# Kernel tuning notes

Measured on AMD Instinct MI355X. Metric: run time of the kernel, lower is better.

The kernel has to match this reference:

```python
import jax, jax.numpy as jnp
import numpy as np

B = 524288
N = 30
BETA = 3.0
MAX_A = 5.0

def setup_inputs() -> dict:
    key = jax.random.key(0)
    ks = jax.random.split(key, 10)
    return {
        "s":   jax.random.normal(ks[0], (B, 10), jnp.float32),
        "a":   jax.random.normal(ks[1], (B, 2), jnp.float32),
        "W1":  jax.random.normal(ks[2], (10, 100), jnp.float32) * 0.3,
        "b1":  jax.random.normal(ks[3], (100,), jnp.float32) * 0.1,
        "W2":  jax.random.normal(ks[4], (100, 30), jnp.float32) * 0.1,
        "b2":  jax.random.normal(ks[5], (30,), jnp.float32) * 0.1,
        "L1":  jax.random.normal(ks[6], (10, 100), jnp.float32) * 0.3,
        "bl1": jax.random.normal(ks[7], (100,), jnp.float32) * 0.1,
        "WL2": jax.random.normal(ks[8], (N, 100, 2), jnp.float32) * 0.1,
        "bL2": jax.random.normal(ks[9], (N, 2), jnp.float32) * 0.1,
    }

def reference(s, a, W1, b1, W2, b2, L1, bl1, WL2, bL2):
    # value branch: relu MLP -> per-centroid values [B, N]
    hv = jax.nn.relu(s @ W1 + b1)
    values = hv @ W2 + b2
    # location branch: relu MLP, then N fused tiny linears -> centroids [B, N, 2]
    hl = jax.nn.relu(s @ L1 + bl1)
    centroids = MAX_A * jnp.tanh(jnp.einsum('bh,nhd->bnd', hl, WL2) + bL2)
    # RBF weights: softmax over negated L2 distance to action, scaled by beta
    diff = centroids - a[:, None, :]          # [B, N, 2]
    dist = jnp.sqrt(jnp.sum(diff * diff, axis=2))  # [B, N]
    w = jax.nn.softmax(-BETA * dist, axis=1)
    # weighted sum of centroid values -> [B, 1]
    return jnp.sum(w * values, axis=1, keepdims=True)
```

## Files before the change

### kernel.cpp

```cpp
#include <hip/hip_runtime.h>
#include <hip/hip_fp16.h>


typedef _Float16 f16x8 __attribute__((ext_vector_type(8)));
typedef __fp16 fp16x2 __attribute__((ext_vector_type(2)));
typedef float f32x16 __attribute__((ext_vector_type(16)));
typedef unsigned u32x2 __attribute__((ext_vector_type(2)));

#define OFF_G1 0
#define OFF_WV 4096
#define OFF_WC 7680
#define TOT_HALVES 14848

__device__ __forceinline__ unsigned pkrtz_relu(float a, float b) {
    fp16x2 v = __builtin_amdgcn_cvt_pkrtz(a, b);
    fp16x2 z = {(__fp16)0.f, (__fp16)0.f};
    fp16x2 r = __builtin_elementwise_max(v, z);
    union { fp16x2 v; unsigned u; } U;
    U.v = r;
    return U.u;
}
__device__ __forceinline__ unsigned pk_rne(float a, float b) {
    union { __half h[2]; unsigned u; } U;
    U.h[0] = __float2half(a);
    U.h[1] = __float2half(b);
    return U.u;
}
__device__ __forceinline__ float tanh_fast(float x) {
    float e = exp2f(2.8853900817779268f * x);
    return 1.f - 2.f * __builtin_amdgcn_rcpf(e + 1.f);
}

__global__ __launch_bounds__(256) void prep_kernel(
    const float* __restrict__ W1, const float* __restrict__ b1,
    const float* __restrict__ W2, const float* __restrict__ b2,
    const float* __restrict__ L1, const float* __restrict__ bl1,
    const float* __restrict__ WL2, const float* __restrict__ bL2,
    unsigned short* __restrict__ ws)
{
    int idx = blockIdx.x * 256 + threadIdx.x;
    if (idx >= TOT_HALVES) return;
    float val = 0.f;

    if (idx < OFF_WV) {
        int r = idx >> 11, t = (idx >> 9) & 3;
        int ln = (idx >> 3) & 63, j = idx & 7;
        int c = 32 * t + (ln & 31);
        int k = (ln >> 5) * 8 + j;
        const float* W  = (r == 0) ? W1 : L1;
        const float* bb = (r == 0) ? b1 : bl1;
        if (c < 100)       val = (k < 10) ? W[k * 100 + c] : ((k == 10) ? bb[c] : 0.f);
        else if (c == 100) val = (k == 10) ? 1.f : 0.f;
    } else if (idx < OFF_WC) {
        int i = idx - OFF_WV;
        int kt = i >> 9, ln = (i >> 3) & 63, j = i & 7;
        int v = ln & 31;
        int n = (v & 0x19) | ((v & 4) >> 1) | ((v & 2) << 1);
        int k = kt * 16 + (ln >> 5) * 8 + j;
        if (n < 30) val = (k < 100) ? W2[k * 30 + n] : ((k == 100) ? b2[n] : 0.f);
    } else {
        int i = idx - OFF_WC;
        int T = i / 3584, rem = i % 3584;
        int kt = rem >> 9, ln = (rem >> 3) & 63, j = rem & 7;
        int row = ln & 31;
        int n = 16 * T + (row >> 1), d = row & 1;
        int k = kt * 16 + (ln >> 5) * 8 + j;
        if (n < 30) val = (k < 100) ? WL2[(n * 100 + k) * 2 + d]
                                    : ((k == 100) ? bL2[n * 2 + d] : 0.f);
    }
    union { __half h; unsigned short u; } cv;
    cv.h = __float2half(val);
    ws[idx] = cv.u;
}

__global__ __launch_bounds__(512, 4) void fused_kernel(
    const float* __restrict__ s, const float* __restrict__ a,
    const unsigned short* __restrict__ ws, float* __restrict__ out)
{
    __shared__ unsigned short lds[TOT_HALVES];
    const int tid  = threadIdx.x;
    const int lane = tid & 63;
    const int wave = tid >> 6;
    const int m32  = lane & 31;
    const int hi   = lane >> 5;
    const int sample = blockIdx.x * 256 + wave * 32 + m32;

    {
        const int4* g4 = (const int4*)ws;
        int4* l4 = (int4*)lds;
        for (int i = tid; i < TOT_HALVES / 8; i += 512) l4[i] = g4[i];
    }

    union Frag { f16x8 v; unsigned u[4]; };
    const f32x16 z16 = {0,0,0,0, 0,0,0,0, 0,0,0,0, 0,0,0,0};

    f16x8 sf;
    {
        Frag H;
        H.u[0] = 0; H.u[1] = 0; H.u[2] = 0; H.u[3] = 0;
        const float2* p = (const float2*)(s + (size_t)sample * 10);
        if (hi == 0) {
            float2 q0 = p[0], q1 = p[1], q2 = p[2], q3 = p[3];
            H.u[0] = pk_rne(q0.x, q0.y);
            H.u[1] = pk_rne(q1.x, q1.y);
            H.u[2] = pk_rne(q2.x, q2.y);
            H.u[3] = pk_rne(q3.x, q3.y);
        } else {
            float2 q4 = p[4];
            H.u[0] = pk_rne(q4.x, q4.y);
            H.u[1] = 0x00003C00u;
        }
        sf = H.v;
    }
    float2 av = ((const float2*)a)[sample];

    __syncthreads();

    f32x16 DV = z16, DC0 = z16, DC1 = z16;

    #pragma unroll
    for (int t = 0; t < 4; ++t) {
        f16x8 aV = *(const f16x8*)(lds + OFF_G1 + (0 * 4 + t) * 512 + lane * 8);
        f16x8 aH = *(const f16x8*)(lds + OFF_G1 + (1 * 4 + t) * 512 + lane * 8);
        f32x16 dv = __builtin_amdgcn_mfma_f32_32x32x16_f16(aV, sf, z16, 0, 0, 0);
        f32x16 dh = __builtin_amdgcn_mfma_f32_32x32x16_f16(aH, sf, z16, 0, 0, 0);

        unsigned qv[8], qh[8];
        #pragma unroll
        for (int q = 0; q < 8; ++q) {
            qv[q] = pkrtz_relu(dv[2 * q], dv[2 * q + 1]);
            qh[q] = pkrtz_relu(dh[2 * q], dh[2 * q + 1]);
        }

        #pragma unroll
        for (int half = 0; half < 2; ++half) {
            const int kt = 2 * t + half;
            if (kt < 7) {
                u32x2 sv0 = __builtin_amdgcn_permlane32_swap(qv[4*half+0], qv[4*half+2], false, false);
                u32x2 sv1 = __builtin_amdgcn_permlane32_swap(qv[4*half+1], qv[4*half+3], false, false);
                u32x2 sh0 = __builtin_amdgcn_permlane32_swap(qh[4*half+0], qh[4*half+2], false, false);
                u32x2 sh1 = __builtin_amdgcn_permlane32_swap(qh[4*half+1], qh[4*half+3], false, false);
                Frag BV, BH;
                BV.u[0] = sv0.x; BV.u[1] = sv1.x; BV.u[2] = sv0.y; BV.u[3] = sv1.y;
                BH.u[0] = sh0.x; BH.u[1] = sh1.x; BH.u[2] = sh0.y; BH.u[3] = sh1.y;

                f16x8 wv  = *(const f16x8*)(lds + OFF_WV + kt * 512 + lane * 8);
                f16x8 wc0 = *(const f16x8*)(lds + OFF_WC + (0 * 7 + kt) * 512 + lane * 8);
                f16x8 wc1 = *(const f16x8*)(lds + OFF_WC + (1 * 7 + kt) * 512 + lane * 8);
                DV  = __builtin_amdgcn_mfma_f32_32x32x16_f16(wv,  BV.v, DV,  0, 0, 0);
                DC0 = __builtin_amdgcn_mfma_f32_32x32x16_f16(wc0, BH.v, DC0, 0, 0, 0);
                DC1 = __builtin_amdgcn_mfma_f32_32x32x16_f16(wc1, BH.v, DC1, 0, 0, 0);
            }
        }
    }

    {
        float num = 0.f, den = 0.f;
        #pragma unroll
        for (int T = 0; T < 2; ++T) {
            #pragma unroll
            for (int q = 0; q < 8; ++q) {
                float cx = (T == 0) ? DC0[2 * q]     : DC1[2 * q];
                float cy = (T == 0) ? DC0[2 * q + 1] : DC1[2 * q + 1];
                float x = 5.f * tanh_fast(cx);
                float y = 5.f * tanh_fast(cy);
                float ex = x - av.x, ey = y - av.y;
                float dist = __builtin_amdgcn_sqrtf(fmaf(ex, ex, ey * ey));
                float wt = exp2f(-4.328085122666891f * dist);
                if (T == 1 && hi == 1 && q >= 6) wt = 0.f;
                num = fmaf(wt, DV[q + 8 * T], num);
                den += wt;
            }
        }
        num += __shfl_xor(num, 32);
        den += __shfl_xor(den, 32);
        if (lane < 32) out[sample] = num * __builtin_amdgcn_rcpf(den);
    }
}

extern "C" void kernel_launch(void* const* d_in, const int* in_sizes, int n_in,
                              void* d_out, int out_size, void* d_ws, size_t ws_size,
                              hipStream_t stream) {
    const float* s   = (const float*)d_in[0];
    const float* a   = (const float*)d_in[1];
    const float* W1  = (const float*)d_in[2];
    const float* b1  = (const float*)d_in[3];
    const float* W2  = (const float*)d_in[4];
    const float* b2  = (const float*)d_in[5];
    const float* L1  = (const float*)d_in[6];
    const float* bl1 = (const float*)d_in[7];
    const float* WL2 = (const float*)d_in[8];
    const float* bL2 = (const float*)d_in[9];
    float* out = (float*)d_out;
    unsigned short* ws = (unsigned short*)d_ws;

    prep_kernel<<<(TOT_HALVES + 255) / 256, 256, 0, stream>>>(
        W1, b1, W2, b2, L1, bl1, WL2, bL2, ws);

    int Btot = out_size;
    int grid = Btot / 256;
    fused_kernel<<<grid, 512, 0, stream>>>(s, a, ws, out);
}
```

Measured before the change: 38.80 us.

## Process two 32-sample tiles per wave to reuse LDS weight fragments

Each wave now handles 64 samples as two independent 32-sample MFMA tiles. Every weight fragment loaded from LDS feeds two MFMAs, and the grid is halved, so the per-block LDS weight copy is paid half as often. The cost is twice the accumulator and fragment registers per wave, with launch bounds relaxed from 4 to 2 blocks per CU, which may lower occupancy.

```diff
diff --git a/kernel.cpp b/kernel.cpp
--- a/kernel.cpp
+++ b/kernel.cpp
@@ -73,7 +73,7 @@
     ws[idx] = cv.u;
 }
 
-__global__ __launch_bounds__(512, 4) void fused_kernel(
+__global__ __launch_bounds__(512, 2) void fused_kernel(
     const float* __restrict__ s, const float* __restrict__ a,
     const unsigned short* __restrict__ ws, float* __restrict__ out)
 {
@@ -83,7 +83,9 @@
     const int wave = tid >> 6;
     const int m32  = lane & 31;
     const int hi   = lane >> 5;
-    const int sample = blockIdx.x * 256 + wave * 32 + m32;
+    const int base = blockIdx.x * 512 + wave * 64;
+    const int sA = base + m32;
+    const int sB = base + 32 + m32;
 
     {
         const int4* g4 = (const int4*)ws;
@@ -94,8 +96,7 @@
     union Frag { f16x8 v; unsigned u[4]; };
     const f32x16 z16 = {0,0,0,0, 0,0,0,0, 0,0,0,0, 0,0,0,0};
 
-    f16x8 sf;
-    {
+    auto loadS = [&](int sample) -> f16x8 {
         Frag H;
         H.u[0] = 0; H.u[1] = 0; H.u[2] = 0; H.u[3] = 0;
         const float2* p = (const float2*)(s + (size_t)sample * 10);
@@ -110,51 +111,76 @@
             H.u[0] = pk_rne(q4.x, q4.y);
             H.u[1] = 0x00003C00u;
         }
-        sf = H.v;
-    }
-    float2 av = ((const float2*)a)[sample];
+        return H.v;
+    };
+    f16x8 sfA = loadS(sA);
+    f16x8 sfB = loadS(sB);
+    float2 avA = ((const float2*)a)[sA];
+    float2 avB = ((const float2*)a)[sB];
 
     __syncthreads();
 
-    f32x16 DV = z16, DC0 = z16, DC1 = z16;
+    f32x16 DVA = z16, DC0A = z16, DC1A = z16;
+    f32x16 DVB = z16, DC0B = z16, DC1B = z16;
 
     #pragma unroll
     for (int t = 0; t < 4; ++t) {
-        f16x8 aV = *(const f16x8*)(lds + OFF_G1 + (0 * 4 + t) * 512 + lane * 8);
-        f16x8 aH = *(const f16x8*)(lds + OFF_G1 + (1 * 4 + t) * 512 + lane * 8);
-        f32x16 dv = __builtin_amdgcn_mfma_f32_32x32x16_f16(aV, sf, z16, 0, 0, 0);
-        f32x16 dh = __builtin_amdgcn_mfma_f32_32x32x16_f16(aH, sf, z16, 0, 0, 0);
-
-        unsigned qv[8], qh[8];
-        #pragma unroll
-        for (int q = 0; q < 8; ++q) {
-            qv[q] = pkrtz_relu(dv[2 * q], dv[2 * q + 1]);
-            qh[q] = pkrtz_relu(dh[2 * q], dh[2 * q + 1]);
+        unsigned qvA[8], qhA[8], qvB[8], qhB[8];
+        {
+            f16x8 aV = *(const f16x8*)(lds + OFF_G1 + (0 * 4 + t) * 512 + lane * 8);
+            f32x16 dvA = __builtin_amdgcn_mfma_f32_32x32x16_f16(aV, sfA, z16, 0, 0, 0);
+            f32x16 dvB = __builtin_amdgcn_mfma_f32_32x32x16_f16(aV, sfB, z16, 0, 0, 0);
+            #pragma unroll
+            for (int q = 0; q < 8; ++q) {
+                qvA[q] = pkrtz_relu(dvA[2 * q], dvA[2 * q + 1]);
+                qvB[q] = pkrtz_relu(dvB[2 * q], dvB[2 * q + 1]);
+            }
+        }
+        {
+            f16x8 aH = *(const f16x8*)(lds + OFF_G1 + (1 * 4 + t) * 512 + lane * 8);
+            f32x16 dhA = __builtin_amdgcn_mfma_f32_32x32x16_f16(aH, sfA, z16, 0, 0, 0);
+            f32x16 dhB = __builtin_amdgcn_mfma_f32_32x32x16_f16(aH, sfB, z16, 0, 0, 0);
+            #pragma unroll
+            for (int q = 0; q < 8; ++q) {
+                qhA[q] = pkrtz_relu(dhA[2 * q], dhA[2 * q + 1]);
+                qhB[q] = pkrtz_relu(dhB[2 * q], dhB[2 * q + 1]);
+            }
         }
 
         #pragma unroll
         for (int half = 0; half < 2; ++half) {
             const int kt = 2 * t + half;
             if (kt < 7) {
-                u32x2 sv0 = __builtin_amdgcn_permlane32_swap(qv[4*half+0], qv[4*half+2], false, false);
-                u32x2 sv1 = __builtin_amdgcn_permlane32_swap(qv[4*half+1], qv[4*half+3], false, false);
-                u32x2 sh0 = __builtin_amdgcn_permlane32_swap(qh[4*half+0], qh[4*half+2], false, false);
-                u32x2 sh1 = __builtin_amdgcn_permlane32_swap(qh[4*half+1], qh[4*half+3], false, false);
-                Frag BV, BH;
-                BV.u[0] = sv0.x; BV.u[1] = sv1.x; BV.u[2] = sv0.y; BV.u[3] = sv1.y;
-                BH.u[0] = sh0.x; BH.u[1] = sh1.x; BH.u[2] = sh0.y; BH.u[3] = sh1.y;
-
-                f16x8 wv  = *(const f16x8*)(lds + OFF_WV + kt * 512 + lane * 8);
+                const int b = half * 4;
+                u32x2 svA0 = __builtin_amdgcn_permlane32_swap(qvA[b+0], qvA[b+2], false, false);
+                u32x2 svA1 = __builtin_amdgcn_permlane32_swap(qvA[b+1], qvA[b+3], false, false);
+                u32x2 shA0 = __builtin_amdgcn_permlane32_swap(qhA[b+0], qhA[b+2], false, false);
+                u32x2 shA1 = __builtin_amdgcn_permlane32_swap(qhA[b+1], qhA[b+3], false, false);
+                u32x2 svB0 = __builtin_amdgcn_permlane32_swap(qvB[b+0], qvB[b+2], false, false);
+                u32x2 svB1 = __builtin_amdgcn_permlane32_swap(qvB[b+1], qvB[b+3], false, false);
+                u32x2 shB0 = __builtin_amdgcn_permlane32_swap(qhB[b+0], qhB[b+2], false, false);
+                u32x2 shB1 = __builtin_amdgcn_permlane32_swap(qhB[b+1], qhB[b+3], false, false);
+                Frag BVA, BHA, BVB, BHB;
+                BVA.u[0] = svA0.x; BVA.u[1] = svA1.x; BVA.u[2] = svA0.y; BVA.u[3] = svA1.y;
+                BHA.u[0] = shA0.x; BHA.u[1] = shA1.x; BHA.u[2] = shA0.y; BHA.u[3] = shA1.y;
+                BVB.u[0] = svB0.x; BVB.u[1] = svB1.x; BVB.u[2] = svB0.y; BVB.u[3] = svB1.y;
+                BHB.u[0] = shB0.x; BHB.u[1] = shB1.x; BHB.u[2] = shB0.y; BHB.u[3] = shB1.y;
+
+                f16x8 wv = *(const f16x8*)(lds + OFF_WV + kt * 512 + lane * 8);
+                DVA = __builtin_amdgcn_mfma_f32_32x32x16_f16(wv, BVA.v, DVA, 0, 0, 0);
+                DVB = __builtin_amdgcn_mfma_f32_32x32x16_f16(wv, BVB.v, DVB, 0, 0, 0);
                 f16x8 wc0 = *(const f16x8*)(lds + OFF_WC + (0 * 7 + kt) * 512 + lane * 8);
+                DC0A = __builtin_amdgcn_mfma_f32_32x32x16_f16(wc0, BHA.v, DC0A, 0, 0, 0);
+                DC0B = __builtin_amdgcn_mfma_f32_32x32x16_f16(wc0, BHB.v, DC0B, 0, 0, 0);
                 f16x8 wc1 = *(const f16x8*)(lds + OFF_WC + (1 * 7 + kt) * 512 + lane * 8);
-                DV  = __builtin_amdgcn_mfma_f32_32x32x16_f16(wv,  BV.v, DV,  0, 0, 0);
-                DC0 = __builtin_amdgcn_mfma_f32_32x32x16_f16(wc0, BH.v, DC0, 0, 0, 0);
-                DC1 = __builtin_amdgcn_mfma_f32_32x32x16_f16(wc1, BH.v, DC1, 0, 0, 0);
+                DC1A = __builtin_amdgcn_mfma_f32_32x32x16_f16(wc1, BHA.v, DC1A, 0, 0, 0);
+                DC1B = __builtin_amdgcn_mfma_f32_32x32x16_f16(wc1, BHB.v, DC1B, 0, 0, 0);
             }
         }
     }
 
-    {
+    auto epi = [&](const f32x16& DV, const f32x16& DC0, const f32x16& DC1,
+                   float2 av, int sample) {
         float num = 0.f, den = 0.f;
         #pragma unroll
         for (int T = 0; T < 2; ++T) {
@@ -175,7 +201,9 @@
         num += __shfl_xor(num, 32);
         den += __shfl_xor(den, 32);
         if (lane < 32) out[sample] = num * __builtin_amdgcn_rcpf(den);
-    }
+    };
+    epi(DVA, DC0A, DC1A, avA, sA);
+    epi(DVB, DC0B, DC1B, avB, sB);
 }
 
 extern "C" void kernel_launch(void* const* d_in, const int* in_sizes, int n_in,
@@ -198,6 +226,6 @@
         W1, b1, W2, b2, L1, bl1, WL2, bL2, ws);
 
     int Btot = out_size;
-    int grid = Btot / 256;
+    int grid = Btot / 512;
     fused_kernel<<<grid, 512, 0, stream>>>(s, a, ws, out);
 }
```

Result: slower. 45.10 us (+16.2%).
